# Performance work log

Measured on AMD Instinct MI355X. Metric: run time of the kernel, lower is better.

Reference implementation:

```python
import jax, jax.numpy as jnp
import numpy as np

N = 50000   # nodes
IN = 128    # in_dim
H = 4       # attn heads
F = 32      # out_feats per head (H*F == IN -> Identity residual)
E = 500000  # edges per edge type
L = 512     # label dim
SLOPE = 0.2 # leaky_relu negative slope


def setup_inputs() -> dict:
    key = jax.random.key(0)
    ks = jax.random.split(key, 12)
    x = jax.random.normal(ks[0], (N, IN), jnp.float32)
    y = jax.random.uniform(ks[1], (N, L), jnp.float32)
    src_p = jax.random.randint(ks[2], (E,), 0, N)
    dst_p = jax.random.randint(ks[3], (E,), 0, N)
    src_s = jax.random.randint(ks[4], (E,), 0, N)
    dst_s = jax.random.randint(ks[5], (E,), 0, N)
    dst_flag = jax.random.randint(ks[6], (N,), 0, 2).astype(bool)
    # shared GAT parameters (share_weight=True)
    W_src = jax.random.normal(ks[7], (H * F, IN), jnp.float32) * 0.05
    b_src = jnp.zeros((H * F,), jnp.float32)
    W_dst = jax.random.normal(ks[8], (H * F, IN), jnp.float32) * 0.05
    b_dst = jnp.zeros((H * F,), jnp.float32)
    attn = jax.random.normal(ks[9], (1, H, F), jnp.float32) * 0.1
    return {"x": x, "y": y, "W_src": W_src, "b_src": b_src, "W_dst": W_dst,
            "b_dst": b_dst, "attn": attn, "src_p": src_p, "dst_p": dst_p,
            "src_s": src_s, "dst_s": dst_s, "dst_flag": dst_flag}


def _edge_softmax(logits, dst):
    # softmax over incoming edges per destination node, per head
    m = jax.ops.segment_max(logits, dst, num_segments=N)          # (N,H)
    ex = jnp.exp(logits - m[dst])
    s = jax.ops.segment_sum(ex, dst, num_segments=N)              # (N,H)
    return ex / s[dst]


def _gat(x, src, dst, W_src, b_src, W_dst, b_dst, attn):
    fs = (x @ W_src.T + b_src).reshape(N, H, F)   # feat_src 'el'
    fd = (x @ W_dst.T + b_dst).reshape(N, H, F)   # feat_dst 'er'
    # u_add_v -> leaky_relu -> dot with attn vector
    e = jax.nn.leaky_relu(fs[src] + fd[dst], SLOPE)               # (E,H,F)
    logits = jnp.einsum('ehf,hf->eh', e, attn[0])                 # (E,H)
    a = _edge_softmax(logits, dst)                                # (E,H)
    # u_mul_e + sum aggregation
    ft = jax.ops.segment_sum(fs[src] * a[:, :, None], dst, num_segments=N)  # (N,H,F)
    rst = ft + x.reshape(N, H, F)  # Identity residual (IN == H*F)
    return rst.mean(axis=1), a.mean(axis=1)       # (N,F), (E,)


def reference(x, y, W_src, b_src, W_dst, b_dst, attn,
              src_p, dst_p, src_s, dst_s, dst_flag):
    h_p, a_p = _gat(x, src_p, dst_p, W_src, b_src, W_dst, b_dst, attn)
    h_s, a_s = _gat(x, src_s, dst_s, W_src, b_src, W_dst, b_dst, attn)
    h = jax.nn.elu(h_p + h_s)                                     # (N,F)
    # label propagation with the (head-averaged) attention coefficients
    yh = (jax.ops.segment_sum(y[src_p] * a_p[:, None], dst_p, num_segments=N)
          + jax.ops.segment_sum(y[src_s] * a_s[:, None], dst_s, num_segments=N))
    norm = jnp.linalg.norm(yh, axis=1, keepdims=True)             # F.normalize, p=2, dim=1
    yh = yh / jnp.maximum(norm, 1e-12)
    y_hat = jnp.where(dst_flag[:, None], y, yh)  # y_hat[dst_flag] = y0
    return h, y_hat
```

## Files before the change

kernel.cpp:

```cpp
#include <hip/hip_runtime.h>

#define NN 50000
#define INDIM 128
#define HH 4
#define FF 32
#define EE 500000
#define LL 512
#define SLOPE 0.2f
#define FSTR 256
#define ELLW 96
#define ELLH 48
#define DSTRIDE 32

#define NB_ZERO  1563
#define NB_WCONV 16
#define NB_CONVY 12500
#define NB_K0    (NB_ZERO + NB_WCONV + 1 + NB_CONVY)
#define NB_SCAT  3907
#define NB_MFMA  3125
#define NB_K1    (NB_SCAT + NB_MFMA)

using bf16x8 = __attribute__((ext_vector_type(8))) short;
using f32x4  = __attribute__((ext_vector_type(4))) float;
using f32x2  = __attribute__((ext_vector_type(2))) float;

static __device__ inline unsigned short f2b(float f) {
    union { float f; unsigned int u; } v;
    v.f = f;
    unsigned int u = v.u;
    u += 0x7FFF + ((u >> 16) & 1);
    return (unsigned short)(u >> 16);
}
static __device__ inline float b2f(unsigned int u16) {
    union { unsigned int u; float f; } v;
    v.u = u16 << 16;
    return v.f;
}
static __device__ inline unsigned char f2e4m3(float f) {
    return (unsigned char)(__builtin_amdgcn_cvt_pk_fp8_f32(f, f, 0u, false) & 0xff);
}

__global__ void k0_kernel(uint4* __restrict__ deg2v,
                          const float* __restrict__ Wsrc, const float* __restrict__ Wdst,
                          unsigned short* __restrict__ wb,
                          const unsigned char* __restrict__ flagbuf, int* __restrict__ mode,
                          const float* __restrict__ y, unsigned char* __restrict__ y8) {
    const int bid = blockIdx.x;
    const int t = threadIdx.x;
    if (bid < NB_ZERO) {
        const int i = bid * 256 + t;
        if (i < NN * DSTRIDE / 4) deg2v[i] = make_uint4(0u, 0u, 0u, 0u);
    } else if (bid < NB_ZERO + NB_WCONV) {
        const int i = (bid - NB_ZERO) * 256 + t;
        const int e = i * 8;
        const int row = e >> 7;
        const int col = e & 127;
        const float* sp = (row < INDIM) ? (Wsrc + (size_t)row * INDIM + col)
                                        : (Wdst + (size_t)(row - INDIM) * INDIM + col);
        const float4 a = reinterpret_cast<const float4*>(sp)[0];
        const float4 b = reinterpret_cast<const float4*>(sp)[1];
        unsigned short o[8] = {f2b(a.x), f2b(a.y), f2b(a.z), f2b(a.w),
                               f2b(b.x), f2b(b.y), f2b(b.z), f2b(b.w)};
        reinterpret_cast<bf16x8*>(wb)[i] = *reinterpret_cast<const bf16x8*>(o);
    } else if (bid == NB_ZERO + NB_WCONV) {
        __shared__ int cnt;
        if (t == 0) cnt = 0;
        __syncthreads();
        int c = 0;
        for (int i = t; i < NN; i += 256)
            if ((i & 3) && flagbuf[i]) c++;
        atomicAdd(&cnt, c);
        __syncthreads();
        if (t == 0) *mode = (cnt == 0) ? 1 : 0;
    } else {
        const int i = (bid - NB_ZERO - NB_WCONV - 1) * 256 + t;
        const float4 a = reinterpret_cast<const float4*>(y)[(size_t)i * 2];
        const float4 b = reinterpret_cast<const float4*>(y)[(size_t)i * 2 + 1];
        unsigned int r0 = 0, r1 = 0;
        r0 = __builtin_amdgcn_cvt_pk_fp8_f32(a.x, a.y, r0, false);
        r0 = __builtin_amdgcn_cvt_pk_fp8_f32(a.z, a.w, r0, true);
        r1 = __builtin_amdgcn_cvt_pk_fp8_f32(b.x, b.y, r1, false);
        r1 = __builtin_amdgcn_cvt_pk_fp8_f32(b.z, b.w, r1, true);
        reinterpret_cast<uint2*>(y8)[i] = make_uint2(r0, r1);
    }
}

__global__ void k1_kernel(const float* __restrict__ xf, const unsigned short* __restrict__ wb,
                          const float* __restrict__ bsrc, const float* __restrict__ bdst,
                          unsigned char* __restrict__ fcat8,
                          const int* __restrict__ src_p, const int* __restrict__ dst_p,
                          const int* __restrict__ src_s, const int* __restrict__ dst_s,
                          int* __restrict__ deg2, int* __restrict__ ell) {
    const int bid = (int)(((unsigned int)blockIdx.x * 7919u) % (unsigned int)NB_K1);
    const int t = threadIdx.x;
    if (bid < NB_SCAT) {
        const int e = bid * 256 + t;
        if (e < 2 * EE) {
            int d, s;
            unsigned int ty;
            if (e < EE) { d = dst_p[e]; s = src_p[e]; ty = 0u; }
            else        { d = dst_s[e - EE]; s = src_s[e - EE]; ty = 1u << 31; }
            const int sub = e & 1;
            const int slot = atomicAdd(&deg2[(size_t)d * DSTRIDE + sub * 16], 1);
            if (slot < ELLH)
                ell[(size_t)d * ELLW + sub * ELLH + slot] = (int)((unsigned int)s | ty);
        }
    } else {
        __shared__ unsigned char st8[16 * 256];
        const int wave = t >> 6;
        const int lane = t & 63;
        const int n0 = (bid - NB_SCAT) * 16;
        const int r = lane & 15;
        const int kb = (lane >> 4) * 8;
        f32x4 acc[4] = {{0.f, 0.f, 0.f, 0.f}, {0.f, 0.f, 0.f, 0.f},
                        {0.f, 0.f, 0.f, 0.f}, {0.f, 0.f, 0.f, 0.f}};
#pragma unroll
        for (int ks = 0; ks < 4; ++ks) {
            const float4 xa = *reinterpret_cast<const float4*>(xf + (size_t)(n0 + r) * INDIM + ks * 32 + kb);
            const float4 xb4 = *reinterpret_cast<const float4*>(xf + (size_t)(n0 + r) * INDIM + ks * 32 + kb + 4);
            unsigned short ao[8] = {f2b(xa.x), f2b(xa.y), f2b(xa.z), f2b(xa.w),
                                    f2b(xb4.x), f2b(xb4.y), f2b(xb4.z), f2b(xb4.w)};
            const bf16x8 a = *reinterpret_cast<const bf16x8*>(ao);
#pragma unroll
            for (int tI = 0; tI < 4; ++tI) {
                const int j = wave * 64 + tI * 16 + r;
                const bf16x8 bf = *reinterpret_cast<const bf16x8*>(wb + (size_t)j * INDIM + ks * 32 + kb);
                acc[tI] = __builtin_amdgcn_mfma_f32_16x16x32_bf16(a, bf, acc[tI], 0, 0, 0);
            }
        }
        const int rowg = (lane >> 4) * 4;
#pragma unroll
        for (int tI = 0; tI < 4; ++tI) {
            const int j = wave * 64 + tI * 16 + r;
            const float bias = (j < INDIM) ? bsrc[j] : bdst[j - INDIM];
#pragma unroll
            for (int q = 0; q < 4; ++q)
                st8[(rowg + q) * 256 + j] = f2e4m3(acc[tI][q] + bias);
        }
        __syncthreads();
        {
            const uint4 v = *reinterpret_cast<const uint4*>(&st8[t * 16]);
            *reinterpret_cast<uint4*>(fcat8 + (size_t)n0 * FSTR + t * 16) = v;
        }
    }
}

__global__ __launch_bounds__(256) void
mega_kernel(const float* __restrict__ x, const float* __restrict__ yf,
            const unsigned char* __restrict__ y8,
            const unsigned char* __restrict__ fcat8,
            const float* __restrict__ attn,
            const int* __restrict__ deg2, const int* __restrict__ ell,
            const void* __restrict__ flagbuf, const int* __restrict__ mode,
            float* __restrict__ hout, float* __restrict__ yhat) {
    const int t = threadIdx.x;
    const int w = t >> 6, l = t & 63;
    const int n = blockIdx.x * 4 + w;
    const int c0 = min(deg2[(size_t)n * DSTRIDE], ELLH);
    const int c1 = min(deg2[(size_t)n * DSTRIDE + 16], ELLH);
    const int cnt = c0 + c1;
    const int base = n * ELLW;
    const int sub = l >> 4, sl = l & 15;

    __shared__ uint2 evL[4][ELLW];
    __shared__ float amL[4][ELLW];
    __shared__ int srcL[4][ELLW];

    const bool flag = (*mode == 1) ? (reinterpret_cast<const int*>(flagbuf)[n] != 0)
                                   : (reinterpret_cast<const unsigned char*>(flagbuf)[n] != 0);

    for (int i = l; i < cnt; i += 64) {
        const int idx = (i < c0) ? i : (ELLH + i - c0);
        srcL[w][i] = ell[base + idx];
    }

    float fdf[8], atv[8];
    {
        const uint2 fdv = *reinterpret_cast<const uint2*>(fcat8 + (size_t)n * FSTR + 128 + sl * 8);
        const f32x2 q0 = __builtin_amdgcn_cvt_pk_f32_fp8(fdv.x, false);
        const f32x2 q1 = __builtin_amdgcn_cvt_pk_f32_fp8(fdv.x, true);
        const f32x2 q2 = __builtin_amdgcn_cvt_pk_f32_fp8(fdv.y, false);
        const f32x2 q3 = __builtin_amdgcn_cvt_pk_f32_fp8(fdv.y, true);
        fdf[0] = q0.x; fdf[1] = q0.y; fdf[2] = q1.x; fdf[3] = q1.y;
        fdf[4] = q2.x; fdf[5] = q2.y; fdf[6] = q3.x; fdf[7] = q3.y;
        const float4 a0 = *reinterpret_cast<const float4*>(attn + sl * 8);
        const float4 a1 = *reinterpret_cast<const float4*>(attn + sl * 8 + 4);
        atv[0] = a0.x; atv[1] = a0.y; atv[2] = a0.z; atv[3] = a0.w;
        atv[4] = a1.x; atv[5] = a1.y; atv[6] = a1.z; atv[7] = a1.w;
    }

    float facP[8] = {0.f, 0.f, 0.f, 0.f, 0.f, 0.f, 0.f, 0.f};
    float facS[8] = {0.f, 0.f, 0.f, 0.f, 0.f, 0.f, 0.f, 0.f};
    float denP = 0.f, denS = 0.f;

#pragma unroll 2
    for (int i = sub; i < cnt; i += 4) {
        const int sv = srcL[w][i];
        const int s = sv & 0x7fffffff;
        const bool tyS = sv < 0;
        const uint2 fsv = *reinterpret_cast<const uint2*>(fcat8 + (size_t)s * FSTR + sl * 8);
        const f32x2 q0 = __builtin_amdgcn_cvt_pk_f32_fp8(fsv.x, false);
        const f32x2 q1 = __builtin_amdgcn_cvt_pk_f32_fp8(fsv.x, true);
        const f32x2 q2 = __builtin_amdgcn_cvt_pk_f32_fp8(fsv.y, false);
        const f32x2 q3 = __builtin_amdgcn_cvt_pk_f32_fp8(fsv.y, true);
        const float fsf[8] = {q0.x, q0.y, q1.x, q1.y, q2.x, q2.y, q3.x, q3.y};
        float v = 0.f;
#pragma unroll
        for (int j = 0; j < 8; ++j) {
            const float xx = fsf[j] + fdf[j];
            v += fmaxf(xx, SLOPE * xx) * atv[j];
        }
        v += __shfl_xor(v, 1);
        v += __shfl_xor(v, 2);
        const float ev = b2f(f2b(__expf(v)));
        const float evP = tyS ? 0.f : ev;
        const float evS = tyS ? ev : 0.f;
#pragma unroll
        for (int j = 0; j < 8; ++j) {
            facP[j] += evP * fsf[j];
            facS[j] += evS * fsf[j];
        }
        denP += ((sl & 3) == 0) ? evP : 0.f;
        denS += ((sl & 3) == 0) ? evS : 0.f;
        const float pu = __shfl_xor(ev, 4);
        if ((sl & 7) == 0)
            reinterpret_cast<unsigned int*>(&evL[w][0])[i * 2 + (sl >> 3)] =
                (unsigned int)f2b(ev) | ((unsigned int)f2b(pu) << 16);
    }

    denP += __shfl_xor(denP, 16); denP += __shfl_xor(denP, 32);
    denS += __shfl_xor(denS, 16); denS += __shfl_xor(denS, 32);

    float dInv[8];
#pragma unroll
    for (int h = 0; h < 4; ++h) {
        const float dp = __shfl(denP, h * 4);
        const float ds_ = __shfl(denS, h * 4);
        dInv[h] = (dp > 0.f) ? 1.f / dp : 0.f;
        dInv[4 + h] = (ds_ > 0.f) ? 1.f / ds_ : 0.f;
    }

    {
#pragma unroll
        for (int j = 0; j < 8; ++j) {
            facP[j] += __shfl_xor(facP[j], 16); facP[j] += __shfl_xor(facP[j], 32);
            facS[j] += __shfl_xor(facS[j], 16); facS[j] += __shfl_xor(facS[j], 32);
        }
        const int h = sl >> 2;
        float sft[8];
#pragma unroll
        for (int j = 0; j < 8; ++j) {
            sft[j] = facP[j] * dInv[h] + facS[j] * dInv[4 + h];
            sft[j] += __shfl_xor(sft[j], 4);
            sft[j] += __shfl_xor(sft[j], 8);
        }
        if (l < 4) {
            const int o = l * 8;
            float xs[8] = {0.f, 0.f, 0.f, 0.f, 0.f, 0.f, 0.f, 0.f};
#pragma unroll
            for (int h2 = 0; h2 < 4; ++h2) {
                const float4 xa = *reinterpret_cast<const float4*>(x + (size_t)n * INDIM + h2 * 32 + o);
                const float4 xb4 = *reinterpret_cast<const float4*>(x + (size_t)n * INDIM + h2 * 32 + o + 4);
                xs[0] += xa.x; xs[1] += xa.y; xs[2] += xa.z; xs[3] += xa.w;
                xs[4] += xb4.x; xs[5] += xb4.y; xs[6] += xb4.z; xs[7] += xb4.w;
            }
            float r[8];
#pragma unroll
            for (int j = 0; j < 8; ++j) {
                const float sacc = 0.25f * sft[j] + 0.5f * xs[j];
                r[j] = sacc > 0.f ? sacc : (__expf(sacc) - 1.f);
            }
            *reinterpret_cast<float4*>(hout + (size_t)n * FF + o) = make_float4(r[0], r[1], r[2], r[3]);
            *reinterpret_cast<float4*>(hout + (size_t)n * FF + o + 4) = make_float4(r[4], r[5], r[6], r[7]);
        }
    }

    if (flag) {
        const float4 a = *reinterpret_cast<const float4*>(yf + (size_t)n * LL + l * 8);
        const float4 b = *reinterpret_cast<const float4*>(yf + (size_t)n * LL + l * 8 + 4);
        *reinterpret_cast<float4*>(yhat + (size_t)n * LL + l * 8) = a;
        *reinterpret_cast<float4*>(yhat + (size_t)n * LL + l * 8 + 4) = b;
        return;
    }

    for (int i = l; i < cnt; i += 64) {
        const int sv = srcL[w][i];
        const int bh = (sv < 0) ? 4 : 0;
        const uint2 e = evL[w][i];
        amL[w][i] = 0.25f * (b2f(e.x & 0xffff) * dInv[bh] + b2f(e.x >> 16) * dInv[bh + 1] +
                             b2f(e.y & 0xffff) * dInv[bh + 2] + b2f(e.y >> 16) * dInv[bh + 3]);
    }

    const int half = l >> 5;
    const int cl = l & 31;
    float acc[16];
#pragma unroll
    for (int j = 0; j < 16; ++j) acc[j] = 0.f;
#pragma unroll 2
    for (int i = half; i < cnt; i += 2) {
        const float am = amL[w][i];
        const int s = srcL[w][i] & 0x7fffffff;
        const uint4 yv = *reinterpret_cast<const uint4*>(y8 + (size_t)s * LL + cl * 16);
        const unsigned int yu[4] = {yv.x, yv.y, yv.z, yv.w};
#pragma unroll
        for (int j = 0; j < 4; ++j) {
            const f32x2 p0 = __builtin_amdgcn_cvt_pk_f32_fp8(yu[j], false);
            const f32x2 p1 = __builtin_amdgcn_cvt_pk_f32_fp8(yu[j], true);
            acc[4 * j + 0] += p0.x * am;
            acc[4 * j + 1] += p0.y * am;
            acc[4 * j + 2] += p1.x * am;
            acc[4 * j + 3] += p1.y * am;
        }
    }
#pragma unroll
    for (int j = 0; j < 16; ++j) acc[j] += __shfl_xor(acc[j], 32);
    float ss = 0.f;
#pragma unroll
    for (int j = 0; j < 16; ++j) ss += acc[j] * acc[j];
    for (int off = 16; off; off >>= 1) ss += __shfl_xor(ss, off);
    const float scale = 1.f / fmaxf(sqrtf(ss), 1e-12f);
    if (half == 0) {
        float* dst = yhat + (size_t)n * LL + cl * 16;
        *reinterpret_cast<float4*>(dst) =
            make_float4(acc[0] * scale, acc[1] * scale, acc[2] * scale, acc[3] * scale);
        *reinterpret_cast<float4*>(dst + 4) =
            make_float4(acc[4] * scale, acc[5] * scale, acc[6] * scale, acc[7] * scale);
        *reinterpret_cast<float4*>(dst + 8) =
            make_float4(acc[8] * scale, acc[9] * scale, acc[10] * scale, acc[11] * scale);
        *reinterpret_cast<float4*>(dst + 12) =
            make_float4(acc[12] * scale, acc[13] * scale, acc[14] * scale, acc[15] * scale);
    }
}

extern "C" void kernel_launch(void* const* d_in, const int* in_sizes, int n_in,
                              void* d_out, int out_size, void* d_ws, size_t ws_size,
                              hipStream_t stream) {
    const float* x    = (const float*)d_in[0];
    const float* y    = (const float*)d_in[1];
    const float* Wsrc = (const float*)d_in[2];
    const float* bsrc = (const float*)d_in[3];
    const float* Wdst = (const float*)d_in[4];
    const float* bdst = (const float*)d_in[5];
    const float* attn = (const float*)d_in[6];
    const int* src_p  = (const int*)d_in[7];
    const int* dst_p  = (const int*)d_in[8];
    const int* src_s  = (const int*)d_in[9];
    const int* dst_s  = (const int*)d_in[10];
    const void* dflag = d_in[11];

    float* out  = (float*)d_out;
    float* hout = out;
    float* yhat = out + (size_t)NN * FF;

    char* base = (char*)d_ws;
    unsigned char*  fcat8 = (unsigned char*)base;
    unsigned char*  y8    = (unsigned char*)(base + 12800000);
    unsigned short* wb    = (unsigned short*)(base + 38400000);
    int*            ell   = (int*)(base + 38500000);
    int*            deg2  = (int*)(base + 57700000);
    int*            mode  = (int*)(base + 64100000);

    k0_kernel<<<NB_K0, 256, 0, stream>>>((uint4*)deg2, Wsrc, Wdst, wb,
                                         (const unsigned char*)dflag, mode, y, y8);

    k1_kernel<<<NB_K1, 256, 0, stream>>>(x, wb, bsrc, bdst, fcat8,
                                         src_p, dst_p, src_s, dst_s, deg2, ell);

    mega_kernel<<<NN / 4, 256, 0, stream>>>(x, y, y8, fcat8, attn, deg2, ell,
                                            dflag, mode, hout, yhat);
}
```

Baseline: 276.8 us.

## Move projection GEMM into first kernel, converting weights to bf16 inline

The weight pre-conversion blocks are removed. The MFMA projection now runs in k0 alongside the zeroing and y-to-fp8 conversion, reading fp32 weights and converting them to bf16 in registers. k1 is left doing only the edge scatter into the ELL lists. This shortens the dependency chain between kernels and balances the work across them. In exchange, every projection block repeats the weight conversion and reads fp32 weights, which doubles weight traffic, though that traffic should mostly hit cache.

```diff
diff --git a/kernel.cpp b/kernel.cpp
--- a/kernel.cpp
+++ b/kernel.cpp
@@ -13,12 +13,10 @@
 #define DSTRIDE 32
 
 #define NB_ZERO  1563
-#define NB_WCONV 16
+#define NB_MFMA  3125
 #define NB_CONVY 12500
-#define NB_K0    (NB_ZERO + NB_WCONV + 1 + NB_CONVY)
+#define NB_K0    (NB_ZERO + 1 + NB_MFMA + NB_CONVY)
 #define NB_SCAT  3907
-#define NB_MFMA  3125
-#define NB_K1    (NB_SCAT + NB_MFMA)
 
 using bf16x8 = __attribute__((ext_vector_type(8))) short;
 using f32x4  = __attribute__((ext_vector_type(4))) float;
@@ -42,27 +40,16 @@
 
 __global__ void k0_kernel(uint4* __restrict__ deg2v,
                           const float* __restrict__ Wsrc, const float* __restrict__ Wdst,
-                          unsigned short* __restrict__ wb,
+                          const float* __restrict__ bsrc, const float* __restrict__ bdst,
+                          const float* __restrict__ xf, unsigned char* __restrict__ fcat8,
                           const unsigned char* __restrict__ flagbuf, int* __restrict__ mode,
                           const float* __restrict__ y, unsigned char* __restrict__ y8) {
-    const int bid = blockIdx.x;
+    const int bid = (int)(((unsigned int)blockIdx.x * 7919u) % (unsigned int)NB_K0);
     const int t = threadIdx.x;
     if (bid < NB_ZERO) {
         const int i = bid * 256 + t;
         if (i < NN * DSTRIDE / 4) deg2v[i] = make_uint4(0u, 0u, 0u, 0u);
-    } else if (bid < NB_ZERO + NB_WCONV) {
-        const int i = (bid - NB_ZERO) * 256 + t;
-        const int e = i * 8;
-        const int row = e >> 7;
-        const int col = e & 127;
-        const float* sp = (row < INDIM) ? (Wsrc + (size_t)row * INDIM + col)
-                                        : (Wdst + (size_t)(row - INDIM) * INDIM + col);
-        const float4 a = reinterpret_cast<const float4*>(sp)[0];
-        const float4 b = reinterpret_cast<const float4*>(sp)[1];
-        unsigned short o[8] = {f2b(a.x), f2b(a.y), f2b(a.z), f2b(a.w),
-                               f2b(b.x), f2b(b.y), f2b(b.z), f2b(b.w)};
-        reinterpret_cast<bf16x8*>(wb)[i] = *reinterpret_cast<const bf16x8*>(o);
-    } else if (bid == NB_ZERO + NB_WCONV) {
+    } else if (bid == NB_ZERO) {
         __shared__ int cnt;
         if (t == 0) cnt = 0;
         __syncthreads();
@@ -72,8 +59,51 @@
         atomicAdd(&cnt, c);
         __syncthreads();
         if (t == 0) *mode = (cnt == 0) ? 1 : 0;
+    } else if (bid < NB_ZERO + 1 + NB_MFMA) {
+        __shared__ unsigned char st8[16 * 256];
+        const int wave = t >> 6;
+        const int lane = t & 63;
+        const int n0 = (bid - NB_ZERO - 1) * 16;
+        const int r = lane & 15;
+        const int kb = (lane >> 4) * 8;
+        f32x4 acc[4] = {{0.f, 0.f, 0.f, 0.f}, {0.f, 0.f, 0.f, 0.f},
+                        {0.f, 0.f, 0.f, 0.f}, {0.f, 0.f, 0.f, 0.f}};
+#pragma unroll
+        for (int ks = 0; ks < 4; ++ks) {
+            const float4 xa = *reinterpret_cast<const float4*>(xf + (size_t)(n0 + r) * INDIM + ks * 32 + kb);
+            const float4 xb4 = *reinterpret_cast<const float4*>(xf + (size_t)(n0 + r) * INDIM + ks * 32 + kb + 4);
+            unsigned short ao[8] = {f2b(xa.x), f2b(xa.y), f2b(xa.z), f2b(xa.w),
+                                    f2b(xb4.x), f2b(xb4.y), f2b(xb4.z), f2b(xb4.w)};
+            const bf16x8 a = *reinterpret_cast<const bf16x8*>(ao);
+#pragma unroll
+            for (int tI = 0; tI < 4; ++tI) {
+                const int j = wave * 64 + tI * 16 + r;
+                const float* Wrow = (j < INDIM) ? (Wsrc + (size_t)j * INDIM)
+                                                : (Wdst + (size_t)(j - INDIM) * INDIM);
+                const float4 wa = *reinterpret_cast<const float4*>(Wrow + ks * 32 + kb);
+                const float4 wv = *reinterpret_cast<const float4*>(Wrow + ks * 32 + kb + 4);
+                unsigned short wo[8] = {f2b(wa.x), f2b(wa.y), f2b(wa.z), f2b(wa.w),
+                                        f2b(wv.x), f2b(wv.y), f2b(wv.z), f2b(wv.w)};
+                const bf16x8 bfr = *reinterpret_cast<const bf16x8*>(wo);
+                acc[tI] = __builtin_amdgcn_mfma_f32_16x16x32_bf16(a, bfr, acc[tI], 0, 0, 0);
+            }
+        }
+        const int rowg = (lane >> 4) * 4;
+#pragma unroll
+        for (int tI = 0; tI < 4; ++tI) {
+            const int j = wave * 64 + tI * 16 + r;
+            const float bias = (j < INDIM) ? bsrc[j] : bdst[j - INDIM];
+#pragma unroll
+            for (int q = 0; q < 4; ++q)
+                st8[(rowg + q) * 256 + j] = f2e4m3(acc[tI][q] + bias);
+        }
+        __syncthreads();
+        {
+            const uint4 v = *reinterpret_cast<const uint4*>(&st8[t * 16]);
+            *reinterpret_cast<uint4*>(fcat8 + (size_t)n0 * FSTR + t * 16) = v;
+        }
     } else {
-        const int i = (bid - NB_ZERO - NB_WCONV - 1) * 256 + t;
+        const int i = (bid - NB_ZERO - 1 - NB_MFMA) * 256 + t;
         const float4 a = reinterpret_cast<const float4*>(y)[(size_t)i * 2];
         const float4 b = reinterpret_cast<const float4*>(y)[(size_t)i * 2 + 1];
         unsigned int r0 = 0, r1 = 0;
@@ -85,63 +115,19 @@
     }
 }
 
-__global__ void k1_kernel(const float* __restrict__ xf, const unsigned short* __restrict__ wb,
-                          const float* __restrict__ bsrc, const float* __restrict__ bdst,
-                          unsigned char* __restrict__ fcat8,
-                          const int* __restrict__ src_p, const int* __restrict__ dst_p,
+__global__ void k1_kernel(const int* __restrict__ src_p, const int* __restrict__ dst_p,
                           const int* __restrict__ src_s, const int* __restrict__ dst_s,
                           int* __restrict__ deg2, int* __restrict__ ell) {
-    const int bid = (int)(((unsigned int)blockIdx.x * 7919u) % (unsigned int)NB_K1);
-    const int t = threadIdx.x;
-    if (bid < NB_SCAT) {
-        const int e = bid * 256 + t;
-        if (e < 2 * EE) {
-            int d, s;
-            unsigned int ty;
-            if (e < EE) { d = dst_p[e]; s = src_p[e]; ty = 0u; }
-            else        { d = dst_s[e - EE]; s = src_s[e - EE]; ty = 1u << 31; }
-            const int sub = e & 1;
-            const int slot = atomicAdd(&deg2[(size_t)d * DSTRIDE + sub * 16], 1);
-            if (slot < ELLH)
-                ell[(size_t)d * ELLW + sub * ELLH + slot] = (int)((unsigned int)s | ty);
-        }
-    } else {
-        __shared__ unsigned char st8[16 * 256];
-        const int wave = t >> 6;
-        const int lane = t & 63;
-        const int n0 = (bid - NB_SCAT) * 16;
-        const int r = lane & 15;
-        const int kb = (lane >> 4) * 8;
-        f32x4 acc[4] = {{0.f, 0.f, 0.f, 0.f}, {0.f, 0.f, 0.f, 0.f},
-                        {0.f, 0.f, 0.f, 0.f}, {0.f, 0.f, 0.f, 0.f}};
-#pragma unroll
-        for (int ks = 0; ks < 4; ++ks) {
-            const float4 xa = *reinterpret_cast<const float4*>(xf + (size_t)(n0 + r) * INDIM + ks * 32 + kb);
-            const float4 xb4 = *reinterpret_cast<const float4*>(xf + (size_t)(n0 + r) * INDIM + ks * 32 + kb + 4);
-            unsigned short ao[8] = {f2b(xa.x), f2b(xa.y), f2b(xa.z), f2b(xa.w),
-                                    f2b(xb4.x), f2b(xb4.y), f2b(xb4.z), f2b(xb4.w)};
-            const bf16x8 a = *reinterpret_cast<const bf16x8*>(ao);
-#pragma unroll
-            for (int tI = 0; tI < 4; ++tI) {
-                const int j = wave * 64 + tI * 16 + r;
-                const bf16x8 bf = *reinterpret_cast<const bf16x8*>(wb + (size_t)j * INDIM + ks * 32 + kb);
-                acc[tI] = __builtin_amdgcn_mfma_f32_16x16x32_bf16(a, bf, acc[tI], 0, 0, 0);
-            }
-        }
-        const int rowg = (lane >> 4) * 4;
-#pragma unroll
-        for (int tI = 0; tI < 4; ++tI) {
-            const int j = wave * 64 + tI * 16 + r;
-            const float bias = (j < INDIM) ? bsrc[j] : bdst[j - INDIM];
-#pragma unroll
-            for (int q = 0; q < 4; ++q)
-                st8[(rowg + q) * 256 + j] = f2e4m3(acc[tI][q] + bias);
-        }
-        __syncthreads();
-        {
-            const uint4 v = *reinterpret_cast<const uint4*>(&st8[t * 16]);
-            *reinterpret_cast<uint4*>(fcat8 + (size_t)n0 * FSTR + t * 16) = v;
-        }
+    const int e = blockIdx.x * 256 + threadIdx.x;
+    if (e < 2 * EE) {
+        int d, s;
+        unsigned int ty;
+        if (e < EE) { d = dst_p[e]; s = src_p[e]; ty = 0u; }
+        else        { d = dst_s[e - EE]; s = src_s[e - EE]; ty = 1u << 31; }
+        const int sub = e & 1;
+        const int slot = atomicAdd(&deg2[(size_t)d * DSTRIDE + sub * 16], 1);
+        if (slot < ELLH)
+            ell[(size_t)d * ELLW + sub * ELLH + slot] = (int)((unsigned int)s | ty);
     }
 }
 
@@ -355,16 +341,14 @@
     char* base = (char*)d_ws;
     unsigned char*  fcat8 = (unsigned char*)base;
     unsigned char*  y8    = (unsigned char*)(base + 12800000);
-    unsigned short* wb    = (unsigned short*)(base + 38400000);
     int*            ell   = (int*)(base + 38500000);
     int*            deg2  = (int*)(base + 57700000);
     int*            mode  = (int*)(base + 64100000);
 
-    k0_kernel<<<NB_K0, 256, 0, stream>>>((uint4*)deg2, Wsrc, Wdst, wb,
+    k0_kernel<<<NB_K0, 256, 0, stream>>>((uint4*)deg2, Wsrc, Wdst, bsrc, bdst, x, fcat8,
                                          (const unsigned char*)dflag, mode, y, y8);
 
-    k1_kernel<<<NB_K1, 256, 0, stream>>>(x, wb, bsrc, bdst, fcat8,
-                                         src_p, dst_p, src_s, dst_s, deg2, ell);
+    k1_kernel<<<NB_SCAT, 256, 0, stream>>>(src_p, dst_p, src_s, dst_s, deg2, ell);
 
     mega_kernel<<<NN / 4, 256, 0, stream>>>(x, y, y8, fcat8, attn, deg2, ell,
                                             dflag, mode, hout, yhat);
```

After: 292.9 us. 5.8% more time.

## Move edge scatter into first kernel and zero degrees with memset

Applied to the files above, without the earlier changes.

Zeroing of the degree array moves from in-kernel blocks to hipMemsetAsync. The edge-to-ELL scatter moves from k1 into k0, where it runs alongside the weight conversion, flag check and y-to-fp8 conversion. k1 becomes a pure MFMA projection kernel. The intent is to overlap the atomic-heavy scatter with the bandwidth-bound y conversion and shorten k1, at the cost of an extra memset launch.

```diff
diff --git a/kernel.cpp b/kernel.cpp
--- a/kernel.cpp
+++ b/kernel.cpp
@@ -12,13 +12,11 @@
 #define ELLH 48
 #define DSTRIDE 32
 
-#define NB_ZERO  1563
+#define NB_SCAT  3907
 #define NB_WCONV 16
 #define NB_CONVY 12500
-#define NB_K0    (NB_ZERO + NB_WCONV + 1 + NB_CONVY)
-#define NB_SCAT  3907
+#define NB_K0    (NB_SCAT + NB_WCONV + 1 + NB_CONVY)
 #define NB_MFMA  3125
-#define NB_K1    (NB_SCAT + NB_MFMA)
 
 using bf16x8 = __attribute__((ext_vector_type(8))) short;
 using f32x4  = __attribute__((ext_vector_type(4))) float;
@@ -40,58 +38,14 @@
     return (unsigned char)(__builtin_amdgcn_cvt_pk_fp8_f32(f, f, 0u, false) & 0xff);
 }
 
-__global__ void k0_kernel(uint4* __restrict__ deg2v,
+__global__ void k0_kernel(const int* __restrict__ src_p, const int* __restrict__ dst_p,
+                          const int* __restrict__ src_s, const int* __restrict__ dst_s,
+                          int* __restrict__ deg2, int* __restrict__ ell,
                           const float* __restrict__ Wsrc, const float* __restrict__ Wdst,
                           unsigned short* __restrict__ wb,
                           const unsigned char* __restrict__ flagbuf, int* __restrict__ mode,
                           const float* __restrict__ y, unsigned char* __restrict__ y8) {
-    const int bid = blockIdx.x;
-    const int t = threadIdx.x;
-    if (bid < NB_ZERO) {
-        const int i = bid * 256 + t;
-        if (i < NN * DSTRIDE / 4) deg2v[i] = make_uint4(0u, 0u, 0u, 0u);
-    } else if (bid < NB_ZERO + NB_WCONV) {
-        const int i = (bid - NB_ZERO) * 256 + t;
-        const int e = i * 8;
-        const int row = e >> 7;
-        const int col = e & 127;
-        const float* sp = (row < INDIM) ? (Wsrc + (size_t)row * INDIM + col)
-                                        : (Wdst + (size_t)(row - INDIM) * INDIM + col);
-        const float4 a = reinterpret_cast<const float4*>(sp)[0];
-        const float4 b = reinterpret_cast<const float4*>(sp)[1];
-        unsigned short o[8] = {f2b(a.x), f2b(a.y), f2b(a.z), f2b(a.w),
-                               f2b(b.x), f2b(b.y), f2b(b.z), f2b(b.w)};
-        reinterpret_cast<bf16x8*>(wb)[i] = *reinterpret_cast<const bf16x8*>(o);
-    } else if (bid == NB_ZERO + NB_WCONV) {
-        __shared__ int cnt;
-        if (t == 0) cnt = 0;
-        __syncthreads();
-        int c = 0;
-        for (int i = t; i < NN; i += 256)
-            if ((i & 3) && flagbuf[i]) c++;
-        atomicAdd(&cnt, c);
-        __syncthreads();
-        if (t == 0) *mode = (cnt == 0) ? 1 : 0;
-    } else {
-        const int i = (bid - NB_ZERO - NB_WCONV - 1) * 256 + t;
-        const float4 a = reinterpret_cast<const float4*>(y)[(size_t)i * 2];
-        const float4 b = reinterpret_cast<const float4*>(y)[(size_t)i * 2 + 1];
-        unsigned int r0 = 0, r1 = 0;
-        r0 = __builtin_amdgcn_cvt_pk_fp8_f32(a.x, a.y, r0, false);
-        r0 = __builtin_amdgcn_cvt_pk_fp8_f32(a.z, a.w, r0, true);
-        r1 = __builtin_amdgcn_cvt_pk_fp8_f32(b.x, b.y, r1, false);
-        r1 = __builtin_amdgcn_cvt_pk_fp8_f32(b.z, b.w, r1, true);
-        reinterpret_cast<uint2*>(y8)[i] = make_uint2(r0, r1);
-    }
-}
-
-__global__ void k1_kernel(const float* __restrict__ xf, const unsigned short* __restrict__ wb,
-                          const float* __restrict__ bsrc, const float* __restrict__ bdst,
-                          unsigned char* __restrict__ fcat8,
-                          const int* __restrict__ src_p, const int* __restrict__ dst_p,
-                          const int* __restrict__ src_s, const int* __restrict__ dst_s,
-                          int* __restrict__ deg2, int* __restrict__ ell) {
-    const int bid = (int)(((unsigned int)blockIdx.x * 7919u) % (unsigned int)NB_K1);
+    const int bid = (int)(((unsigned int)blockIdx.x * 7919u) % (unsigned int)NB_K0);
     const int t = threadIdx.x;
     if (bid < NB_SCAT) {
         const int e = bid * 256 + t;
@@ -105,43 +59,80 @@
             if (slot < ELLH)
                 ell[(size_t)d * ELLW + sub * ELLH + slot] = (int)((unsigned int)s | ty);
         }
+    } else if (bid < NB_SCAT + NB_WCONV) {
+        const int i = (bid - NB_SCAT) * 256 + t;
+        const int e = i * 8;
+        const int row = e >> 7;
+        const int col = e & 127;
+        const float* sp = (row < INDIM) ? (Wsrc + (size_t)row * INDIM + col)
+                                        : (Wdst + (size_t)(row - INDIM) * INDIM + col);
+        const float4 a = reinterpret_cast<const float4*>(sp)[0];
+        const float4 b = reinterpret_cast<const float4*>(sp)[1];
+        unsigned short o[8] = {f2b(a.x), f2b(a.y), f2b(a.z), f2b(a.w),
+                               f2b(b.x), f2b(b.y), f2b(b.z), f2b(b.w)};
+        reinterpret_cast<bf16x8*>(wb)[i] = *reinterpret_cast<const bf16x8*>(o);
+    } else if (bid == NB_SCAT + NB_WCONV) {
+        __shared__ int cnt;
+        if (t == 0) cnt = 0;
+        __syncthreads();
+        int c = 0;
+        for (int i = t; i < NN; i += 256)
+            if ((i & 3) && flagbuf[i]) c++;
+        atomicAdd(&cnt, c);
+        __syncthreads();
+        if (t == 0) *mode = (cnt == 0) ? 1 : 0;
     } else {
-        __shared__ unsigned char st8[16 * 256];
-        const int wave = t >> 6;
-        const int lane = t & 63;
-        const int n0 = (bid - NB_SCAT) * 16;
-        const int r = lane & 15;
-        const int kb = (lane >> 4) * 8;
-        f32x4 acc[4] = {{0.f, 0.f, 0.f, 0.f}, {0.f, 0.f, 0.f, 0.f},
-                        {0.f, 0.f, 0.f, 0.f}, {0.f, 0.f, 0.f, 0.f}};
-#pragma unroll
-        for (int ks = 0; ks < 4; ++ks) {
-            const float4 xa = *reinterpret_cast<const float4*>(xf + (size_t)(n0 + r) * INDIM + ks * 32 + kb);
-            const float4 xb4 = *reinterpret_cast<const float4*>(xf + (size_t)(n0 + r) * INDIM + ks * 32 + kb + 4);
-            unsigned short ao[8] = {f2b(xa.x), f2b(xa.y), f2b(xa.z), f2b(xa.w),
-                                    f2b(xb4.x), f2b(xb4.y), f2b(xb4.z), f2b(xb4.w)};
-            const bf16x8 a = *reinterpret_cast<const bf16x8*>(ao);
-#pragma unroll
-            for (int tI = 0; tI < 4; ++tI) {
-                const int j = wave * 64 + tI * 16 + r;
-                const bf16x8 bf = *reinterpret_cast<const bf16x8*>(wb + (size_t)j * INDIM + ks * 32 + kb);
-                acc[tI] = __builtin_amdgcn_mfma_f32_16x16x32_bf16(a, bf, acc[tI], 0, 0, 0);
-            }
-        }
-        const int rowg = (lane >> 4) * 4;
+        const int i = (bid - NB_SCAT - NB_WCONV - 1) * 256 + t;
+        const float4 a = reinterpret_cast<const float4*>(y)[(size_t)i * 2];
+        const float4 b = reinterpret_cast<const float4*>(y)[(size_t)i * 2 + 1];
+        unsigned int r0 = 0, r1 = 0;
+        r0 = __builtin_amdgcn_cvt_pk_fp8_f32(a.x, a.y, r0, false);
+        r0 = __builtin_amdgcn_cvt_pk_fp8_f32(a.z, a.w, r0, true);
+        r1 = __builtin_amdgcn_cvt_pk_fp8_f32(b.x, b.y, r1, false);
+        r1 = __builtin_amdgcn_cvt_pk_fp8_f32(b.z, b.w, r1, true);
+        reinterpret_cast<uint2*>(y8)[i] = make_uint2(r0, r1);
+    }
+}
+
+__global__ void k1_kernel(const float* __restrict__ xf, const unsigned short* __restrict__ wb,
+                          const float* __restrict__ bsrc, const float* __restrict__ bdst,
+                          unsigned char* __restrict__ fcat8) {
+    __shared__ unsigned char st8[16 * 256];
+    const int t = threadIdx.x;
+    const int wave = t >> 6;
+    const int lane = t & 63;
+    const int n0 = blockIdx.x * 16;
+    const int r = lane & 15;
+    const int kb = (lane >> 4) * 8;
+    f32x4 acc[4] = {{0.f, 0.f, 0.f, 0.f}, {0.f, 0.f, 0.f, 0.f},
+                    {0.f, 0.f, 0.f, 0.f}, {0.f, 0.f, 0.f, 0.f}};
+#pragma unroll
+    for (int ks = 0; ks < 4; ++ks) {
+        const float4 xa = *reinterpret_cast<const float4*>(xf + (size_t)(n0 + r) * INDIM + ks * 32 + kb);
+        const float4 xb4 = *reinterpret_cast<const float4*>(xf + (size_t)(n0 + r) * INDIM + ks * 32 + kb + 4);
+        unsigned short ao[8] = {f2b(xa.x), f2b(xa.y), f2b(xa.z), f2b(xa.w),
+                                f2b(xb4.x), f2b(xb4.y), f2b(xb4.z), f2b(xb4.w)};
+        const bf16x8 a = *reinterpret_cast<const bf16x8*>(ao);
 #pragma unroll
         for (int tI = 0; tI < 4; ++tI) {
             const int j = wave * 64 + tI * 16 + r;
-            const float bias = (j < INDIM) ? bsrc[j] : bdst[j - INDIM];
-#pragma unroll
-            for (int q = 0; q < 4; ++q)
-                st8[(rowg + q) * 256 + j] = f2e4m3(acc[tI][q] + bias);
-        }
-        __syncthreads();
-        {
-            const uint4 v = *reinterpret_cast<const uint4*>(&st8[t * 16]);
-            *reinterpret_cast<uint4*>(fcat8 + (size_t)n0 * FSTR + t * 16) = v;
-        }
+            const bf16x8 bf = *reinterpret_cast<const bf16x8*>(wb + (size_t)j * INDIM + ks * 32 + kb);
+            acc[tI] = __builtin_amdgcn_mfma_f32_16x16x32_bf16(a, bf, acc[tI], 0, 0, 0);
+        }
+    }
+    const int rowg = (lane >> 4) * 4;
+#pragma unroll
+    for (int tI = 0; tI < 4; ++tI) {
+        const int j = wave * 64 + tI * 16 + r;
+        const float bias = (j < INDIM) ? bsrc[j] : bdst[j - INDIM];
+#pragma unroll
+        for (int q = 0; q < 4; ++q)
+            st8[(rowg + q) * 256 + j] = f2e4m3(acc[tI][q] + bias);
+    }
+    __syncthreads();
+    {
+        const uint4 v = *reinterpret_cast<const uint4*>(&st8[t * 16]);
+        *reinterpret_cast<uint4*>(fcat8 + (size_t)n0 * FSTR + t * 16) = v;
     }
 }
 
@@ -360,11 +351,13 @@
     int*            deg2  = (int*)(base + 57700000);
     int*            mode  = (int*)(base + 64100000);
 
-    k0_kernel<<<NB_K0, 256, 0, stream>>>((uint4*)deg2, Wsrc, Wdst, wb,
+    hipMemsetAsync(deg2, 0, (size_t)NN * DSTRIDE * sizeof(int), stream);
+
+    k0_kernel<<<NB_K0, 256, 0, stream>>>(src_p, dst_p, src_s, dst_s, deg2, ell,
+                                         Wsrc, Wdst, wb,
                                          (const unsigned char*)dflag, mode, y, y8);
 
-    k1_kernel<<<NB_K1, 256, 0, stream>>>(x, wb, bsrc, bdst, fcat8,
-                                         src_p, dst_p, src_s, dst_s, deg2, ell);
+    k1_kernel<<<NB_MFMA, 256, 0, stream>>>(x, wb, bsrc, bdst, fcat8);
 
     mega_kernel<<<NN / 4, 256, 0, stream>>>(x, y, y8, fcat8, attn, deg2, ell,
                                             dflag, mode, hout, yhat);
```

Result: slower. 284.3 us (+2.7%).
